# Performance work log

Measured on AMD Instinct MI355X. Metric: run time of the kernel, lower is better.

Reference implementation:

```python
import jax, jax.numpy as jnp
import numpy as np

NUM_ANCHORS = 5
NUM_CLASSES = 20


def setup_inputs() -> dict:
    key = jax.random.key(0)
    k1, k2, k3, k4 = jax.random.split(key, 4)
    N, H, W, M = 64, 52, 52, 32
    img = 1664
    x = jax.random.normal(k1, (N, NUM_ANCHORS * (5 + NUM_CLASSES), H, W), jnp.float32)
    anchors = jnp.array([[1.08, 1.19], [3.42, 4.41], [6.63, 11.38],
                         [9.42, 5.11], [16.62, 10.52]], jnp.float32)
    # valid gt boxes in xyxy pixel coords
    xy = jax.random.uniform(k2, (N, M, 2), jnp.float32) * (img * 0.8)
    wh = jax.random.uniform(k3, (N, M, 2), jnp.float32) * (img * 0.2) + 1.0
    gt_boxes = jnp.concatenate([xy, xy + wh], axis=-1)
    gt_labels = jax.random.randint(k4, (N, M), 0, NUM_CLASSES)
    return dict(x=x, anchors=anchors, gt_boxes=gt_boxes, gt_labels=gt_labels,
                img_h=img, img_w=img)


def _format_outputs(x, anchors, img_h, img_w):
    # x: [N, A*(5+C), H, W] -> (coords [N,HW,A,4] (x,y,w,h), obj [N,HW,A], scores [N,HW,A,C])
    N, _, H, W = x.shape
    A = anchors.shape[0]
    t = x.reshape(N, A, 5 + NUM_CLASSES, H, W).transpose(0, 3, 4, 1, 2)  # [N,H,W,A,5+C]
    c_x = jnp.arange(W, dtype=x.dtype) * (img_w / W)
    c_y = jnp.arange(H, dtype=x.dtype) * (img_h / H)
    b_x = jax.nn.sigmoid(t[..., 0]) + c_x[None, None, :, None]   # [N,H,W,A]
    b_y = jax.nn.sigmoid(t[..., 1]) + c_y[None, :, None, None]
    b_w = (img_w / W) * anchors[:, 0] * jnp.exp(t[..., 2])
    b_h = (img_h / H) * anchors[:, 1] * jnp.exp(t[..., 3])
    coords = jnp.stack([b_x, b_y, b_w, b_h], axis=-1).reshape(N, H * W, A, 4)
    b_o = jax.nn.sigmoid(t[..., 4]).reshape(N, H * W, A)
    scores = t[..., 5:].reshape(N, H * W, A, NUM_CLASSES)
    return coords, b_o, scores


def reference(x, anchors, gt_boxes, gt_labels, img_h, img_w):
    coords, b_o, scores = _format_outputs(x, anchors, img_h, img_w)
    # pred_boxes[..., 2:] += pred_boxes[..., :2]  (xywh -> xyxy)
    boxes = jnp.concatenate([coords[..., :2], coords[..., :2] + coords[..., 2:]], axis=-1)  # [N,HW,A,4]
    # box_iou: pred [N,HW,A,1,4] vs gt [N,1,1,M,4] -> [N,HW,A,M]
    p = boxes[..., None, :]
    g = gt_boxes[:, None, None, :, :]
    lt = jnp.maximum(p[..., :2], g[..., :2])
    rb = jnp.minimum(p[..., 2:], g[..., 2:])
    whi = jnp.clip(rb - lt, 0.0)
    inter = whi[..., 0] * whi[..., 1]
    area_p = (boxes[..., 2] - boxes[..., 0]) * (boxes[..., 3] - boxes[..., 1])
    area_g = (gt_boxes[..., 2] - gt_boxes[..., 0]) * (gt_boxes[..., 3] - gt_boxes[..., 1])
    iou = inter / (area_p[..., None] + area_g[:, None, None, :] - inter)   # [N,HW,A,M]

    cell_sel = iou.max(axis=(2, 3)) > 0.0                 # [N,HW]
    best_a = jnp.argmax(iou.max(axis=3), axis=2)          # [N,HW] best anchor per cell
    iou_best = jnp.take_along_axis(iou, best_a[..., None, None], axis=2)[:, :, 0, :]  # [N,HW,M]
    max_iou = iou_best.max(axis=-1)                       # [N,HW]
    gt_idx = jnp.argmax(iou_best, axis=-1)                # [N,HW]

    sel_box = jnp.take_along_axis(boxes, best_a[..., None, None], axis=2)[:, :, 0, :]   # [N,HW,4]
    sel_o = jnp.take_along_axis(b_o, best_a[..., None], axis=2)[:, :, 0]                # [N,HW]
    sel_sc = jnp.take_along_axis(scores, best_a[..., None, None], axis=2)[:, :, 0, :]   # [N,HW,C]
    g_box = jnp.take_along_axis(gt_boxes, gt_idx[..., None], axis=1)                    # [N,HW,4]
    g_lab = jnp.take_along_axis(gt_labels, gt_idx, axis=1)                              # [N,HW]

    m = cell_sel.astype(x.dtype)
    objectness_loss = (jnp.sum(m * (sel_o - max_iou) ** 2)
                       + 0.5 * jnp.sum((1.0 - m) * b_o.max(axis=2) ** 2))
    bbox_loss = (jnp.sum(m * jnp.sum((sel_box[..., :2] - g_box[..., :2]) ** 2, axis=-1))
                 + jnp.sum(m * jnp.sum((jnp.sqrt(sel_box[..., 2:]) - jnp.sqrt(g_box[..., 2:])) ** 2, axis=-1)))
    logp = jax.nn.log_softmax(sel_sc, axis=-1)
    ce = -jnp.take_along_axis(logp, g_lab[..., None], axis=-1)[..., 0]
    clf_loss = jnp.sum(m * ce)
    return jnp.stack([objectness_loss, bbox_loss, clf_loss])
```

## Files before the change

kernel.cpp:

```cpp
#include <hip/hip_runtime.h>
#include <math.h>

#define A_ 5
#define C_ 20
#define N_ 64
#define H_ 52
#define W_ 52
#define HW_ (H_ * W_)
#define M_ 32
#define CH_ (A_ * (5 + C_))
#define CPB 64
#define NBX ((HW_ + CPB - 1) / CPB)
#define NBLK (NBX * N_)

__global__ __launch_bounds__(64) void yolo_main(
    const float* __restrict__ x,
    const float* __restrict__ anchors,
    const float* __restrict__ gt,
    const int* __restrict__ glab,
    const void* img_h_p, const void* img_w_p,
    float* __restrict__ ws)
{
    const int lane = threadIdx.x;
    const int n    = blockIdx.y;
    const int cell = blockIdx.x * CPB + lane;
    const bool valid = cell < HW_;

    int ibw = *(const int*)img_w_p;
    float img_w = (ibw > 0 && ibw < 1000000) ? (float)ibw : *(const float*)img_w_p;
    int ibh = *(const int*)img_h_p;
    float img_h = (ibh > 0 && ibh < 1000000) ? (float)ibh : *(const float*)img_h_p;
    const float sx = img_w / (float)W_;
    const float sy = img_h / (float)H_;

    float obj = 0.f, bbx = 0.f, clf = 0.f;

    if (valid) {
        const size_t base = (size_t)n * CH_ * HW_ + cell;

        float t[A_][5];
        #pragma unroll
        for (int a = 0; a < A_; ++a)
            #pragma unroll
            for (int v = 0; v < 5; ++v)
                t[a][v] = x[base + (size_t)(a * 25 + v) * HW_];

        const int wi = cell % W_;
        const int hi = cell / W_;

        float X1[A_], Y1[A_], X2[A_], Y2[A_], AP[A_], OVv[A_];
        #pragma unroll
        for (int a = 0; a < A_; ++a) {
            float ax = anchors[2 * a];
            float ay = anchors[2 * a + 1];
            float bx = 1.f / (1.f + __expf(-t[a][0])) + (float)wi * sx;
            float by = 1.f / (1.f + __expf(-t[a][1])) + (float)hi * sy;
            float bw = sx * ax * __expf(t[a][2]);
            float bh = sy * ay * __expf(t[a][3]);
            X1[a] = bx; Y1[a] = by; X2[a] = bx + bw; Y2[a] = by + bh;
            AP[a] = (X2[a] - X1[a]) * (Y2[a] - Y1[a]);
            OVv[a] = 1.f / (1.f + __expf(-t[a][4]));
        }

        float BIv[A_] = {0.f, 0.f, 0.f, 0.f, 0.f};
        float BUv[A_] = {1.f, 1.f, 1.f, 1.f, 1.f};
        int   BMv[A_] = {0, 0, 0, 0, 0};
        const float4* gtv = (const float4*)(gt + (size_t)n * M_ * 4);
        #pragma unroll 8
        for (int m = 0; m < M_; ++m) {
            float4 g = gtv[m];
            float area = (g.z - g.x) * (g.w - g.y);
            #pragma unroll
            for (int a = 0; a < A_; ++a) {
                float wq = fminf(X2[a], g.z) - fmaxf(X1[a], g.x);
                float hq = fminf(Y2[a], g.w) - fmaxf(Y1[a], g.y);
                wq = fmaxf(wq, 0.f);
                hq = fmaxf(hq, 0.f);
                float inter = wq * hq;
                float uni = AP[a] + area - inter;
                if (inter * BUv[a] > BIv[a] * uni) {
                    BIv[a] = inter; BUv[a] = uni; BMv[a] = m;
                }
            }
        }

        float Bi = BIv[0], Bu = BUv[0], O = OVv[0];
        float wx1 = X1[0], wy1 = Y1[0], wx2 = X2[0], wy2 = Y2[0];
        int Ba = 0, Bm = BMv[0];
        float bomax = OVv[0];
        #pragma unroll
        for (int a = 1; a < A_; ++a) {
            bomax = fmaxf(bomax, OVv[a]);
            if (BIv[a] * Bu > Bi * BUv[a]) {
                Bi = BIv[a]; Bu = BUv[a]; O = OVv[a];
                wx1 = X1[a]; wy1 = Y1[a]; wx2 = X2[a]; wy2 = Y2[a];
                Ba = a; Bm = BMv[a];
            }
        }

        if (Bi > 0.f) {
            float d = O - Bi / Bu;
            obj = d * d;

            float4 g = ((const float4*)gt)[n * M_ + Bm];
            int lab = glab[n * M_ + Bm];
            float d0 = wx1 - g.x;
            float d1 = wy1 - g.y;
            float d2 = sqrtf(wx2) - sqrtf(g.z);
            float d3 = sqrtf(wy2) - sqrtf(g.w);
            bbx = d0 * d0 + d1 * d1 + d2 * d2 + d3 * d3;

            const size_t sb = base + (size_t)(Ba * 25 + 5) * HW_;
            float sc[C_];
            #pragma unroll
            for (int j = 0; j < C_; ++j)
                sc[j] = x[sb + (size_t)j * HW_];
            float mx = sc[0];
            #pragma unroll
            for (int j = 1; j < C_; ++j) mx = fmaxf(mx, sc[j]);
            float se = 0.f, scl = sc[0];
            #pragma unroll
            for (int j = 0; j < C_; ++j) {
                se += __expf(sc[j] - mx);
                scl = (j == lab) ? sc[j] : scl;
            }
            clf = mx + __logf(se) - scl;
        } else {
            obj = 0.5f * bomax * bomax;
        }
    }

    #pragma unroll
    for (int off = 32; off > 0; off >>= 1) {
        obj += __shfl_down(obj, off, 64);
        bbx += __shfl_down(bbx, off, 64);
        clf += __shfl_down(clf, off, 64);
    }
    if (lane == 0) {
        const int bid = blockIdx.y * gridDim.x + blockIdx.x;
        ws[0 * NBLK + bid] = obj;
        ws[1 * NBLK + bid] = bbx;
        ws[2 * NBLK + bid] = clf;
    }
}

__global__ __launch_bounds__(1024) void yolo_reduce(
    const float* __restrict__ ws, float* __restrict__ out)
{
    __shared__ float s_red[16][3];
    const int tid = threadIdx.x;
    float o = 0.f, b = 0.f, c = 0.f;
    for (int e = tid; e < NBLK; e += 1024) {
        o += ws[0 * NBLK + e];
        b += ws[1 * NBLK + e];
        c += ws[2 * NBLK + e];
    }
    #pragma unroll
    for (int off = 32; off > 0; off >>= 1) {
        o += __shfl_down(o, off, 64);
        b += __shfl_down(b, off, 64);
        c += __shfl_down(c, off, 64);
    }
    const int wid = tid >> 6;
    if ((tid & 63) == 0) {
        s_red[wid][0] = o; s_red[wid][1] = b; s_red[wid][2] = c;
    }
    __syncthreads();
    if (tid == 0) {
        float oo = 0.f, bb = 0.f, cc = 0.f;
        #pragma unroll
        for (int w = 0; w < 16; ++w) {
            oo += s_red[w][0]; bb += s_red[w][1]; cc += s_red[w][2];
        }
        out[0] = oo; out[1] = bb; out[2] = cc;
    }
}

extern "C" void kernel_launch(void* const* d_in, const int* in_sizes, int n_in,
                              void* d_out, int out_size, void* d_ws, size_t ws_size,
                              hipStream_t stream) {
    (void)in_sizes; (void)n_in; (void)out_size; (void)ws_size;
    const float* x    = (const float*)d_in[0];
    const float* anch = (const float*)d_in[1];
    const float* gt   = (const float*)d_in[2];
    const int*   gl   = (const int*)d_in[3];
    const void*  ih   = d_in[4];
    const void*  iw   = d_in[5];
    float* out = (float*)d_out;
    float* ws  = (float*)d_ws;

    dim3 grid(NBX, N_);
    yolo_main<<<grid, dim3(64), 0, stream>>>(x, anch, gt, gl, ih, iw, ws);
    yolo_reduce<<<1, 1024, 0, stream>>>(ws, out);
}
```

Baseline: 141.1 us.

## Split each cell's anchors and class scores across two threads

Each grid cell is now handled by a pair of threads. One thread takes anchors 0-2 and the other takes anchors 3-4, and the pair merges its best anchor with xor shuffles. The 20 class scores are split between the two threads, and log-softmax is combined through shuffles. Blocks grow to 256 threads with a shared-memory reduction per block. This doubles thread-level parallelism and shortens the serial IoU loop per thread, at the cost of extra shuffles, some divergence and padding work on the second thread.

```diff
diff --git a/kernel.cpp b/kernel.cpp
--- a/kernel.cpp
+++ b/kernel.cpp
@@ -9,11 +9,11 @@
 #define HW_ (H_ * W_)
 #define M_ 32
 #define CH_ (A_ * (5 + C_))
-#define CPB 64
-#define NBX ((HW_ + CPB - 1) / CPB)
+#define CPBLK 128
+#define NBX ((HW_ + CPBLK - 1) / CPBLK)
 #define NBLK (NBX * N_)
 
-__global__ __launch_bounds__(64) void yolo_main(
+__global__ __launch_bounds__(256) void yolo_main(
     const float* __restrict__ x,
     const float* __restrict__ anchors,
     const float* __restrict__ gt,
@@ -21,9 +21,11 @@
     const void* img_h_p, const void* img_w_p,
     float* __restrict__ ws)
 {
-    const int lane = threadIdx.x;
+    const int tid  = threadIdx.x;
+    const int sub  = tid & 1;
+    const int p    = tid >> 1;
     const int n    = blockIdx.y;
-    const int cell = blockIdx.x * CPB + lane;
+    const int cell = blockIdx.x * CPBLK + p;
     const bool valid = cell < HW_;
 
     int ibw = *(const int*)img_w_p;
@@ -36,97 +38,137 @@
     float obj = 0.f, bbx = 0.f, clf = 0.f;
 
     if (valid) {
+        const int a0 = sub ? 3 : 0;
         const size_t base = (size_t)n * CH_ * HW_ + cell;
 
-        float t[A_][5];
-        #pragma unroll
-        for (int a = 0; a < A_; ++a)
+        float t[3][5];
+        #pragma unroll
+        for (int i = 0; i < 2; ++i)
             #pragma unroll
             for (int v = 0; v < 5; ++v)
-                t[a][v] = x[base + (size_t)(a * 25 + v) * HW_];
+                t[i][v] = x[base + (size_t)((a0 + i) * 25 + v) * HW_];
+        #pragma unroll
+        for (int v = 0; v < 5; ++v)
+            t[2][v] = (sub == 0) ? x[base + (size_t)(2 * 25 + v) * HW_] : 0.f;
 
         const int wi = cell % W_;
         const int hi = cell / W_;
 
-        float X1[A_], Y1[A_], X2[A_], Y2[A_], AP[A_], OVv[A_];
-        #pragma unroll
-        for (int a = 0; a < A_; ++a) {
-            float ax = anchors[2 * a];
-            float ay = anchors[2 * a + 1];
-            float bx = 1.f / (1.f + __expf(-t[a][0])) + (float)wi * sx;
-            float by = 1.f / (1.f + __expf(-t[a][1])) + (float)hi * sy;
-            float bw = sx * ax * __expf(t[a][2]);
-            float bh = sy * ay * __expf(t[a][3]);
-            X1[a] = bx; Y1[a] = by; X2[a] = bx + bw; Y2[a] = by + bh;
-            AP[a] = (X2[a] - X1[a]) * (Y2[a] - Y1[a]);
-            OVv[a] = 1.f / (1.f + __expf(-t[a][4]));
-        }
-
-        float BIv[A_] = {0.f, 0.f, 0.f, 0.f, 0.f};
-        float BUv[A_] = {1.f, 1.f, 1.f, 1.f, 1.f};
-        int   BMv[A_] = {0, 0, 0, 0, 0};
+        float X1[3], Y1[3], X2[3], Y2[3], AP[3], OVv[3];
+        #pragma unroll
+        for (int i = 0; i < 3; ++i) {
+            int ai = a0 + i;
+            ai = (ai > 4) ? 4 : ai;
+            float ax = anchors[2 * ai];
+            float ay = anchors[2 * ai + 1];
+            float bx = 1.f / (1.f + __expf(-t[i][0])) + (float)wi * sx;
+            float by = 1.f / (1.f + __expf(-t[i][1])) + (float)hi * sy;
+            float bw = sx * ax * __expf(t[i][2]);
+            float bh = sy * ay * __expf(t[i][3]);
+            X1[i] = bx; Y1[i] = by; X2[i] = bx + bw; Y2[i] = by + bh;
+            AP[i] = (X2[i] - X1[i]) * (Y2[i] - Y1[i]);
+            OVv[i] = 1.f / (1.f + __expf(-t[i][4]));
+        }
+        if (sub) {
+            X1[2] = Y1[2] = X2[2] = Y2[2] = 0.f;
+            AP[2] = 0.f;
+            OVv[2] = -1e30f;
+        }
+
+        float BIv[3] = {0.f, 0.f, 0.f};
+        float BUv[3] = {1.f, 1.f, 1.f};
+        int   BMv[3] = {0, 0, 0};
         const float4* gtv = (const float4*)(gt + (size_t)n * M_ * 4);
         #pragma unroll 8
         for (int m = 0; m < M_; ++m) {
             float4 g = gtv[m];
             float area = (g.z - g.x) * (g.w - g.y);
             #pragma unroll
-            for (int a = 0; a < A_; ++a) {
-                float wq = fminf(X2[a], g.z) - fmaxf(X1[a], g.x);
-                float hq = fminf(Y2[a], g.w) - fmaxf(Y1[a], g.y);
+            for (int i = 0; i < 3; ++i) {
+                float wq = fminf(X2[i], g.z) - fmaxf(X1[i], g.x);
+                float hq = fminf(Y2[i], g.w) - fmaxf(Y1[i], g.y);
                 wq = fmaxf(wq, 0.f);
                 hq = fmaxf(hq, 0.f);
                 float inter = wq * hq;
-                float uni = AP[a] + area - inter;
-                if (inter * BUv[a] > BIv[a] * uni) {
-                    BIv[a] = inter; BUv[a] = uni; BMv[a] = m;
+                float uni = AP[i] + area - inter;
+                if (inter * BUv[i] > BIv[i] * uni) {
+                    BIv[i] = inter; BUv[i] = uni; BMv[i] = m;
                 }
             }
         }
 
-        float Bi = BIv[0], Bu = BUv[0], O = OVv[0];
-        float wx1 = X1[0], wy1 = Y1[0], wx2 = X2[0], wy2 = Y2[0];
-        int Ba = 0, Bm = BMv[0];
-        float bomax = OVv[0];
-        #pragma unroll
-        for (int a = 1; a < A_; ++a) {
-            bomax = fmaxf(bomax, OVv[a]);
-            if (BIv[a] * Bu > Bi * BUv[a]) {
-                Bi = BIv[a]; Bu = BUv[a]; O = OVv[a];
-                wx1 = X1[a]; wy1 = Y1[a]; wx2 = X2[a]; wy2 = Y2[a];
-                Ba = a; Bm = BMv[a];
+        float Li = BIv[0], Lu = BUv[0], Lo = OVv[0];
+        float lx1 = X1[0], ly1 = Y1[0], lx2 = X2[0], ly2 = Y2[0];
+        int   La = a0, Lm = BMv[0];
+        float lbomax = OVv[0];
+        #pragma unroll
+        for (int i = 1; i < 3; ++i) {
+            lbomax = fmaxf(lbomax, OVv[i]);
+            if (BIv[i] * Lu > Li * BUv[i]) {
+                Li = BIv[i]; Lu = BUv[i]; Lo = OVv[i];
+                lx1 = X1[i]; ly1 = Y1[i]; lx2 = X2[i]; ly2 = Y2[i];
+                La = a0 + i; Lm = BMv[i];
             }
         }
 
+        float pi_ = __shfl_xor(Li, 1, 64);
+        float pu_ = __shfl_xor(Lu, 1, 64);
+        float po_ = __shfl_xor(Lo, 1, 64);
+        float px1 = __shfl_xor(lx1, 1, 64);
+        float py1 = __shfl_xor(ly1, 1, 64);
+        float px2 = __shfl_xor(lx2, 1, 64);
+        float py2 = __shfl_xor(ly2, 1, 64);
+        int   pa_ = __shfl_xor(La, 1, 64);
+        int   pm_ = __shfl_xor(Lm, 1, 64);
+        float pbm = __shfl_xor(lbomax, 1, 64);
+
+        bool ownWins = sub ? (Li * pu_ > pi_ * Lu)
+                           : !(pi_ * Lu > Li * pu_);
+        float Bi = ownWins ? Li  : pi_;
+        float Bu = ownWins ? Lu  : pu_;
+        float O  = ownWins ? Lo  : po_;
+        float wx1 = ownWins ? lx1 : px1;
+        float wy1 = ownWins ? ly1 : py1;
+        float wx2 = ownWins ? lx2 : px2;
+        float wy2 = ownWins ? ly2 : py2;
+        int   Ba = ownWins ? La : pa_;
+        int   Bm = ownWins ? Lm : pm_;
+        float bomax = fmaxf(lbomax, pbm);
+
         if (Bi > 0.f) {
-            float d = O - Bi / Bu;
-            obj = d * d;
-
-            float4 g = ((const float4*)gt)[n * M_ + Bm];
-            int lab = glab[n * M_ + Bm];
-            float d0 = wx1 - g.x;
-            float d1 = wy1 - g.y;
-            float d2 = sqrtf(wx2) - sqrtf(g.z);
-            float d3 = sqrtf(wy2) - sqrtf(g.w);
-            bbx = d0 * d0 + d1 * d1 + d2 * d2 + d3 * d3;
-
             const size_t sb = base + (size_t)(Ba * 25 + 5) * HW_;
-            float sc[C_];
-            #pragma unroll
-            for (int j = 0; j < C_; ++j)
-                sc[j] = x[sb + (size_t)j * HW_];
+            const int lab = glab[n * M_ + Bm];
+            float sc[10];
+            #pragma unroll
+            for (int jj = 0; jj < 10; ++jj)
+                sc[jj] = x[sb + (size_t)(2 * jj + sub) * HW_];
             float mx = sc[0];
             #pragma unroll
-            for (int j = 1; j < C_; ++j) mx = fmaxf(mx, sc[j]);
-            float se = 0.f, scl = sc[0];
-            #pragma unroll
-            for (int j = 0; j < C_; ++j) {
-                se += __expf(sc[j] - mx);
-                scl = (j == lab) ? sc[j] : scl;
+            for (int jj = 1; jj < 10; ++jj) mx = fmaxf(mx, sc[jj]);
+            mx = fmaxf(mx, __shfl_xor(mx, 1, 64));
+            float se = 0.f;
+            #pragma unroll
+            for (int jj = 0; jj < 10; ++jj) se += __expf(sc[jj] - mx);
+            se += __shfl_xor(se, 1, 64);
+            float scl = -INFINITY;
+            #pragma unroll
+            for (int jj = 0; jj < 10; ++jj)
+                scl = (2 * jj + sub == lab) ? sc[jj] : scl;
+            scl = fmaxf(scl, __shfl_xor(scl, 1, 64));
+
+            if (sub == 0) {
+                float d = O - Bi / Bu;
+                obj = d * d;
+                float4 g = ((const float4*)gt)[n * M_ + Bm];
+                float d0 = wx1 - g.x;
+                float d1 = wy1 - g.y;
+                float d2 = sqrtf(wx2) - sqrtf(g.z);
+                float d3 = sqrtf(wy2) - sqrtf(g.w);
+                bbx = d0 * d0 + d1 * d1 + d2 * d2 + d3 * d3;
+                clf = mx + __logf(se) - scl;
             }
-            clf = mx + __logf(se) - scl;
         } else {
-            obj = 0.5f * bomax * bomax;
+            if (sub == 0) obj = 0.5f * bomax * bomax;
         }
     }
 
@@ -136,11 +178,22 @@
         bbx += __shfl_down(bbx, off, 64);
         clf += __shfl_down(clf, off, 64);
     }
-    if (lane == 0) {
+    __shared__ float s_red[4][3];
+    if ((tid & 63) == 0) {
+        const int wid = tid >> 6;
+        s_red[wid][0] = obj; s_red[wid][1] = bbx; s_red[wid][2] = clf;
+    }
+    __syncthreads();
+    if (tid == 0) {
+        float oo = 0.f, bs = 0.f, cc = 0.f;
+        #pragma unroll
+        for (int w = 0; w < 4; ++w) {
+            oo += s_red[w][0]; bs += s_red[w][1]; cc += s_red[w][2];
+        }
         const int bid = blockIdx.y * gridDim.x + blockIdx.x;
-        ws[0 * NBLK + bid] = obj;
-        ws[1 * NBLK + bid] = bbx;
-        ws[2 * NBLK + bid] = clf;
+        ws[0 * NBLK + bid] = oo;
+        ws[1 * NBLK + bid] = bs;
+        ws[2 * NBLK + bid] = cc;
     }
 }
 
@@ -190,6 +243,6 @@
     float* ws  = (float*)d_ws;
 
     dim3 grid(NBX, N_);
-    yolo_main<<<grid, dim3(64), 0, stream>>>(x, anch, gt, gl, ih, iw, ws);
+    yolo_main<<<grid, dim3(256), 0, stream>>>(x, anch, gt, gl, ih, iw, ws);
     yolo_reduce<<<1, 1024, 0, stream>>>(ws, out);
 }
```

Result: slower. 149.3 us (+5.8%).
